# Performance work log

Hardware: AMD Instinct MI355X
Metric: run time of the kernel (lower is better)

## Reference

```python
import jax, jax.numpy as jnp
import numpy as np

N = 100000
E = 1600000
NFEAT = 128
NHID = 16
HEADS = 4
NCLASS = 40
NEG_SLOPE = 0.2
BN_EPS = 1e-5


def setup_inputs() -> dict:
    key = jax.random.key(0)
    ks = jax.random.split(key, 16)
    HC = NHID * HEADS  # 64
    x = jax.random.normal(ks[0], (N, NFEAT), dtype=jnp.float32)
    edge_index = jax.random.randint(ks[1], (2, E), 0, N, dtype=jnp.int64)
    def glorot(k, shape, fan_in):
        return jax.random.normal(k, shape, dtype=jnp.float32) * (1.0 / np.sqrt(fan_in))
    return {
        "x": x,
        "edge_index": edge_index,
        # layer 1: GATConv(NFEAT -> NHID, heads=HEADS, concat=True)
        "W1": glorot(ks[2], (NFEAT, HC), NFEAT),
        "att_src1": glorot(ks[3], (HEADS, NHID), NHID),
        "att_dst1": glorot(ks[4], (HEADS, NHID), NHID),
        "bias1": jnp.zeros((HC,), dtype=jnp.float32),
        # BatchNorm1d(HC), eval mode (running stats)
        "bn_gamma": jnp.ones((HC,), dtype=jnp.float32),
        "bn_beta": jnp.zeros((HC,), dtype=jnp.float32),
        "bn_mean": jax.random.normal(ks[5], (HC,), dtype=jnp.float32) * 0.1,
        "bn_var": jax.random.uniform(ks[6], (HC,), dtype=jnp.float32, minval=0.5, maxval=1.5),
        # layer 2: GATConv(HC -> NCLASS, heads=1, concat=False)
        "W2": glorot(ks[7], (HC, NCLASS), HC),
        "att_src2": glorot(ks[8], (1, NCLASS), NCLASS),
        "att_dst2": glorot(ks[9], (1, NCLASS), NCLASS),
        "bias2": jnp.zeros((NCLASS,), dtype=jnp.float32),
    }


def gat_conv(x, src, dst, W, att_src, att_dst, bias, concat):
    """PyG GATConv (eval; self-loops assumed already appended to src/dst)."""
    H, C = att_src.shape
    n = x.shape[0]
    h = (x @ W).reshape(n, H, C)                         # [N,H,C]
    a_s = (h * att_src[None]).sum(-1)                    # [N,H]
    a_d = (h * att_dst[None]).sum(-1)                    # [N,H]
    alpha = jax.nn.leaky_relu(a_s[src] + a_d[dst], NEG_SLOPE)  # [Et,H]
    # segment softmax over incoming edges of each destination node
    amax = jax.ops.segment_max(alpha, dst, num_segments=n)    # [N,H]
    ex = jnp.exp(alpha - amax[dst])
    denom = jax.ops.segment_sum(ex, dst, num_segments=n)
    coef = ex / denom[dst]                               # [Et,H]
    msg = h[src] * coef[:, :, None]                      # [Et,H,C]
    out = jax.ops.segment_sum(msg, dst, num_segments=n)  # [N,H,C]
    out = out.reshape(n, H * C) if concat else out.mean(axis=1)
    return out + bias


def reference(x, edge_index, W1, att_src1, att_dst1, bias1,
              bn_gamma, bn_beta, bn_mean, bn_var,
              W2, att_src2, att_dst2, bias2):
    n = x.shape[0]
    loops = jnp.arange(n, dtype=edge_index.dtype)
    src = jnp.concatenate([edge_index[0], loops])
    dst = jnp.concatenate([edge_index[1], loops])
    h = gat_conv(x, src, dst, W1, att_src1, att_dst1, bias1, concat=True)
    h = (h - bn_mean) * jax.lax.rsqrt(bn_var + BN_EPS) * bn_gamma + bn_beta
    h = jax.nn.relu(h)  # dropout is identity in eval
    out = gat_conv(h, src, dst, W2, att_src2, att_dst2, bias2, concat=False)
    return out
```

## Files before the change

kernel.cpp:

```cpp
#include <hip/hip_runtime.h>
#include <hip/hip_bf16.h>
#include <hip/hip_fp16.h>

#define NFEAT  128
#define HC     64
#define HEADS  4
#define NHID   16
#define NCLASS 40
#define NEG    0.2f
#define BN_EPS 1e-5f

#define BK_SH   9
#define CHUNK   8192
#define STAGE   12288

typedef _Float16 half8_t __attribute__((ext_vector_type(8)));
typedef _Float16 half4_t __attribute__((ext_vector_type(4)));
typedef float    f32x4_t __attribute__((ext_vector_type(4)));

__device__ __forceinline__ float leaky(float a) { return (a > 0.f) ? a : NEG * a; }

__global__ __launch_bounds__(256) void k_gemm1(
    const float* __restrict__ x, const float* __restrict__ W1,
    const float* __restrict__ att_s, const float* __restrict__ att_d,
    __half* __restrict__ h1, float* __restrict__ as1, float* __restrict__ ad1,
    int n)
{
    const int wave = threadIdx.x >> 6, lane = threadIdx.x & 63;
    const int quad = lane >> 4, l16 = lane & 15;

    half8_t bfrag[4][4];
    #pragma unroll
    for (int ks = 0; ks < 4; ++ks)
        #pragma unroll
        for (int ct = 0; ct < 4; ++ct)
            #pragma unroll
            for (int j = 0; j < 8; ++j)
                bfrag[ks][ct][j] =
                    (_Float16)W1[(ks * 32 + quad * 8 + j) * HC + ct * 16 + l16];

    float avs[4], avd[4];
    #pragma unroll
    for (int ct = 0; ct < 4; ++ct) {
        avs[ct] = att_s[ct * 16 + l16];
        avd[ct] = att_d[ct * 16 + l16];
    }

    const int nslab = (n + 15) >> 4;
    for (int slab = blockIdx.x * 4 + wave; slab < nslab; slab += gridDim.x * 4) {
        const int rowbase = slab * 16;
        const int arow = min(rowbase + l16, n - 1);
        const float* xp = x + (size_t)arow * NFEAT;

        f32x4_t acc[4] = {{0.f,0.f,0.f,0.f},{0.f,0.f,0.f,0.f},
                          {0.f,0.f,0.f,0.f},{0.f,0.f,0.f,0.f}};
        #pragma unroll
        for (int ks = 0; ks < 4; ++ks) {
            const float4 xa = *(const float4*)(xp + ks * 32 + quad * 8);
            const float4 xb = *(const float4*)(xp + ks * 32 + quad * 8 + 4);
            half8_t af;
            af[0] = (_Float16)xa.x; af[1] = (_Float16)xa.y;
            af[2] = (_Float16)xa.z; af[3] = (_Float16)xa.w;
            af[4] = (_Float16)xb.x; af[5] = (_Float16)xb.y;
            af[6] = (_Float16)xb.z; af[7] = (_Float16)xb.w;
            #pragma unroll
            for (int ct = 0; ct < 4; ++ct)
                acc[ct] = __builtin_amdgcn_mfma_f32_16x16x32_f16(
                    af, bfrag[ks][ct], acc[ct], 0, 0, 0);
        }

        #pragma unroll
        for (int reg = 0; reg < 4; ++reg) {
            const int row = rowbase + quad * 4 + reg;
            const bool valid = row < n;

            float4 ps, pd;
            ps.x = acc[0][reg] * avs[0]; pd.x = acc[0][reg] * avd[0];
            ps.y = acc[1][reg] * avs[1]; pd.y = acc[1][reg] * avd[1];
            ps.z = acc[2][reg] * avs[2]; pd.z = acc[2][reg] * avd[2];
            ps.w = acc[3][reg] * avs[3]; pd.w = acc[3][reg] * avd[3];
            #pragma unroll
            for (int off = 8; off >= 1; off >>= 1) {
                ps.x += __shfl_xor(ps.x, off, 64); pd.x += __shfl_xor(pd.x, off, 64);
                ps.y += __shfl_xor(ps.y, off, 64); pd.y += __shfl_xor(pd.y, off, 64);
                ps.z += __shfl_xor(ps.z, off, 64); pd.z += __shfl_xor(pd.z, off, 64);
                ps.w += __shfl_xor(ps.w, off, 64); pd.w += __shfl_xor(pd.w, off, 64);
            }
            if (valid) {
                #pragma unroll
                for (int ct = 0; ct < 4; ++ct)
                    h1[(size_t)row * HC + ct * 16 + l16] =
                        __float2half_rn(acc[ct][reg]);
                if (l16 == 0) {
                    *(float4*)(as1 + (size_t)row * HEADS) = ps;
                    *(float4*)(ad1 + (size_t)row * HEADS) = pd;
                }
            }
        }
    }
}

__global__ __launch_bounds__(512) void k_hist(
    const int* __restrict__ edst, int* __restrict__ hist, int E, int nbk)
{
    __shared__ int lh[256];
    const int w = blockIdx.x, t = threadIdx.x;
    for (int i = t; i < nbk; i += 512) lh[i] = 0;
    __syncthreads();
    const int lo = w * CHUNK, hi = min(E, lo + CHUNK);
    for (int e = lo + 4 * t; e < hi; e += 4 * 512) {
        const int4 d4 = *(const int4*)(edst + e);
        atomicAdd(&lh[d4.x >> BK_SH], 1);
        atomicAdd(&lh[d4.y >> BK_SH], 1);
        atomicAdd(&lh[d4.z >> BK_SH], 1);
        atomicAdd(&lh[d4.w >> BK_SH], 1);
    }
    __syncthreads();
    for (int i = t; i < nbk; i += 512) hist[(size_t)w * nbk + i] = lh[i];
}

__global__ __launch_bounds__(256) void k_colscan(
    int* __restrict__ hist, int* __restrict__ colsum, int nbk, int nw)
{
    __shared__ int wred[4];
    const int b = blockIdx.x, t = threadIdx.x;
    const int lane = t & 63, w = t >> 6;
    const int v = (t < nw) ? hist[(size_t)t * nbk + b] : 0;
    int sc = v;
    #pragma unroll
    for (int off = 1; off < 64; off <<= 1) {
        int u = __shfl_up(sc, off, 64);
        if (lane >= off) sc += u;
    }
    if (lane == 63) wred[w] = sc;
    __syncthreads();
    if (t == 0) { int a = 0; for (int i = 0; i < 4; ++i) { int xx = wred[i]; wred[i] = a; a += xx; } }
    __syncthreads();
    const int excl = sc - v + wred[w];
    if (t < nw) hist[(size_t)t * nbk + b] = excl;
    if (t == nw - 1) colsum[b] = excl + v;
}

__global__ __launch_bounds__(256) void k_bscan(
    const int* __restrict__ colsum, int* __restrict__ bstart, int nbk, int E)
{
    __shared__ int wred[4];
    const int t = threadIdx.x, lane = t & 63, w = t >> 6;
    const int v = (t < nbk) ? colsum[t] : 0;
    int sc = v;
    #pragma unroll
    for (int off = 1; off < 64; off <<= 1) {
        int u = __shfl_up(sc, off, 64);
        if (lane >= off) sc += u;
    }
    if (lane == 63) wred[w] = sc;
    __syncthreads();
    if (t == 0) { int a = 0; for (int i = 0; i < 4; ++i) { int xx = wred[i]; wred[i] = a; a += xx; } }
    __syncthreads();
    if (t < nbk) bstart[t] = sc - v + wred[w];
    if (t == 0) bstart[nbk] = E;
}

__global__ __launch_bounds__(512) void k_scatter(
    const int* __restrict__ esrc, const int* __restrict__ edst,
    const int* __restrict__ hist, const int* __restrict__ bstart,
    int2* __restrict__ pairs, int E, int nbk)
{
    __shared__ int cur[256];
    const int w = blockIdx.x, t = threadIdx.x;
    for (int i = t; i < nbk; i += 512)
        cur[i] = bstart[i] + hist[(size_t)w * nbk + i];
    __syncthreads();
    const int lo = w * CHUNK, hi = min(E, lo + CHUNK);
    for (int e = lo + 4 * t; e < hi; e += 4 * 512) {
        const int4 s4 = *(const int4*)(esrc + e);
        const int4 d4 = *(const int4*)(edst + e);
        int pos;
        pos = atomicAdd(&cur[d4.x >> BK_SH], 1); pairs[pos] = make_int2(s4.x, d4.x);
        pos = atomicAdd(&cur[d4.y >> BK_SH], 1); pairs[pos] = make_int2(s4.y, d4.y);
        pos = atomicAdd(&cur[d4.z >> BK_SH], 1); pairs[pos] = make_int2(s4.z, d4.z);
        pos = atomicAdd(&cur[d4.w >> BK_SH], 1); pairs[pos] = make_int2(s4.w, d4.w);
    }
}

__global__ __launch_bounds__(512) void k_build(
    const int2* __restrict__ pairs, const int* __restrict__ bstart,
    int* __restrict__ rowptr, int* __restrict__ csr, int n, int nbk)
{
    __shared__ int cnt[512];
    __shared__ int cur[512];
    __shared__ int stage[STAGE];
    __shared__ int wred[8];
    const int b = blockIdx.x, t = threadIdx.x;
    const int base = bstart[b], eend = bstart[b + 1], m = eend - base;
    const int n0 = b << BK_SH;
    const int nn = min(512, n - n0);

    cnt[t] = 0;
    __syncthreads();
    for (int e = base + t; e < eend; e += 512)
        atomicAdd(&cnt[pairs[e].y - n0], 1);
    __syncthreads();

    const int v = cnt[t];
    const int lane = t & 63, w = t >> 6;
    int sc = v;
    #pragma unroll
    for (int off = 1; off < 64; off <<= 1) {
        int u = __shfl_up(sc, off, 64);
        if (lane >= off) sc += u;
    }
    if (lane == 63) wred[w] = sc;
    __syncthreads();
    if (t == 0) { int a = 0; for (int i = 0; i < 8; ++i) { int xx = wred[i]; wred[i] = a; a += xx; } }
    __syncthreads();
    const int excl = sc - v + wred[w];
    cur[t] = excl;
    if (t < nn) rowptr[n0 + t] = base + excl + v;
    __syncthreads();

    for (int e = base + t; e < eend; e += 512) {
        const int2 p = pairs[e];
        const int loc = atomicAdd(&cur[p.y - n0], 1);
        if (loc < STAGE) stage[loc] = p.x;
        else             csr[base + loc] = p.x;
    }
    __syncthreads();
    const int lim = min(m, STAGE);
    for (int i = t; i < lim; i += 512) csr[base + i] = stage[i];
}

__global__ __launch_bounds__(256, 4) void k_agg1(
    const int* __restrict__ csr, const int* __restrict__ rowptr,
    const __half* __restrict__ h1, const float* __restrict__ as1,
    const float* __restrict__ ad1,
    const float* __restrict__ bias1, const float* __restrict__ gamma,
    const float* __restrict__ beta, const float* __restrict__ mean,
    const float* __restrict__ var,
    const float* __restrict__ W2, const float* __restrict__ ats2,
    const float* __restrict__ atd2,
    __half* __restrict__ g, float* __restrict__ as2o, float* __restrict__ ad2o,
    int n)
{
    __shared__ _Float16 sWh[NCLASS * HC];
    __shared__ float sh[16][68];
    __shared__ float sE[16][4][20];
    for (int i = threadIdx.x; i < NCLASS * HC; i += 256) sWh[i] = (_Float16)W2[i];
    __syncthreads();

    const int gi = threadIdx.x >> 4;
    const int q  = threadIdx.x & 15;
    const int myh = q >> 2;
    const unsigned nclamp = (unsigned)(n - 1);

    const float4 b1v = *(const float4*)(bias1 + 4 * q);
    const float4 gmv = *(const float4*)(gamma + 4 * q);
    const float4 vrv = *(const float4*)(var   + 4 * q);
    const float4 mnv = *(const float4*)(mean  + 4 * q);
    const float4 btv = *(const float4*)(beta  + 4 * q);
    float4 scv, shv;
    scv.x = gmv.x * rsqrtf(vrv.x + BN_EPS);
    scv.y = gmv.y * rsqrtf(vrv.y + BN_EPS);
    scv.z = gmv.z * rsqrtf(vrv.z + BN_EPS);
    scv.w = gmv.w * rsqrtf(vrv.w + BN_EPS);
    shv.x = btv.x - mnv.x * scv.x;
    shv.y = btv.y - mnv.y * scv.y;
    shv.z = btv.z - mnv.z * scv.z;
    shv.w = btv.w - mnv.w * scv.w;
    float4 at2 = {0.f, 0.f, 0.f, 0.f}, dt2 = {0.f, 0.f, 0.f, 0.f};
    if (q < 10) {
        at2 = *(const float4*)(ats2 + 4 * q);
        dt2 = *(const float4*)(atd2 + 4 * q);
    }

    for (int node0 = blockIdx.x * 16; node0 < n; node0 += gridDim.x * 16) {
        const int node = node0 + gi;
        if (node >= n) continue;

        const float4 adv = *(const float4*)(ad1 + node * HEADS);
        const float4 sv4 = *(const float4*)(as1 + node * HEADS);
        float4 eself;
        eself.x = __expf(leaky(sv4.x + adv.x));
        eself.y = __expf(leaky(sv4.y + adv.y));
        eself.z = __expf(leaky(sv4.z + adv.z));
        eself.w = __expf(leaky(sv4.w + adv.w));
        const float es = (myh == 0) ? eself.x : (myh == 1) ? eself.y
                       : (myh == 2) ? eself.z : eself.w;

        float4 acc;
        {
            const half4_t hv = *(const half4_t*)(h1 + (size_t)node * HC + 4 * q);
            acc.x = es * (float)hv[0]; acc.y = es * (float)hv[1];
            acc.z = es * (float)hv[2]; acc.w = es * (float)hv[3];
        }
        float4 dpart = {0.f, 0.f, 0.f, 0.f};

        const int start = (node == 0) ? 0 : rowptr[node - 1];
        const int end   = rowptr[node];

        for (int base = start; base < end; base += 16) {
            const int m = end - base;
            const int* cb = csr + base;

            const int myraw = cb[min(q, m - 1)];
            int idxs[16];
            #pragma unroll
            for (int e = 0; e < 16; ++e) idxs[e] = cb[e];

            half4_t wreg[16];
            #pragma unroll
            for (int e = 0; e < 16; ++e) {
                const unsigned off =
                    (min((unsigned)idxs[e], nclamp) << 7) + ((unsigned)q << 3);
                wreg[e] = *(const half4_t*)((const char*)h1 + off);
            }
            const float4 s4 =
                *(const float4*)(as1 + (size_t)min((unsigned)myraw, nclamp) * HEADS);
            __builtin_amdgcn_sched_barrier(0);

            const bool val = q < m;
            float4 ea;
            ea.x = val ? __expf(leaky(s4.x + adv.x)) : 0.f;
            ea.y = val ? __expf(leaky(s4.y + adv.y)) : 0.f;
            ea.z = val ? __expf(leaky(s4.z + adv.z)) : 0.f;
            ea.w = val ? __expf(leaky(s4.w + adv.w)) : 0.f;
            dpart.x += ea.x; dpart.y += ea.y;
            dpart.z += ea.z; dpart.w += ea.w;
            sE[gi][0][q] = ea.x;
            sE[gi][1][q] = ea.y;
            sE[gi][2][q] = ea.z;
            sE[gi][3][q] = ea.w;

            float eev[16];
            *(float4*)&eev[0]  = *(const float4*)&sE[gi][myh][0];
            *(float4*)&eev[4]  = *(const float4*)&sE[gi][myh][4];
            *(float4*)&eev[8]  = *(const float4*)&sE[gi][myh][8];
            *(float4*)&eev[12] = *(const float4*)&sE[gi][myh][12];

            #pragma unroll
            for (int e = 0; e < 16; ++e) {
                const float ee = eev[e];
                acc.x = fmaf((float)wreg[e][0], ee, acc.x);
                acc.y = fmaf((float)wreg[e][1], ee, acc.y);
                acc.z = fmaf((float)wreg[e][2], ee, acc.z);
                acc.w = fmaf((float)wreg[e][3], ee, acc.w);
            }
        }

        #pragma unroll
        for (int off = 8; off >= 1; off >>= 1) {
            dpart.x += __shfl_xor(dpart.x, off, 64);
            dpart.y += __shfl_xor(dpart.y, off, 64);
            dpart.z += __shfl_xor(dpart.z, off, 64);
            dpart.w += __shfl_xor(dpart.w, off, 64);
        }
        const float den = es + ((myh == 0) ? dpart.x : (myh == 1) ? dpart.y
                               : (myh == 2) ? dpart.z : dpart.w);
        const float rden = 1.f / den;

        float4 v;
        v.x = fmaxf(fmaf(acc.x * rden + b1v.x, scv.x, shv.x), 0.f);
        v.y = fmaxf(fmaf(acc.y * rden + b1v.y, scv.y, shv.y), 0.f);
        v.z = fmaxf(fmaf(acc.z * rden + b1v.z, scv.z, shv.z), 0.f);
        v.w = fmaxf(fmaf(acc.w * rden + b1v.w, scv.w, shv.w), 0.f);
        *(float4*)&sh[gi][4 * q] = v;

        float4 gacc = {0.f, 0.f, 0.f, 0.f};
        if (q < 10) {
            #pragma unroll 8
            for (int k = 0; k < HC; ++k) {
                const float hk = sh[gi][k];
                const half4_t wv = *(const half4_t*)&sWh[k * NCLASS + 4 * q];
                gacc.x = fmaf(hk, (float)wv[0], gacc.x);
                gacc.y = fmaf(hk, (float)wv[1], gacc.y);
                gacc.z = fmaf(hk, (float)wv[2], gacc.z);
                gacc.w = fmaf(hk, (float)wv[3], gacc.w);
            }
        }
        __half2 p0 = __float22half2_rn({gacc.x, gacc.y});
        __half2 p1 = __float22half2_rn({gacc.z, gacc.w});
        float2 packed; *(__half2*)&packed.x = p0; *(__half2*)&packed.y = p1;
        *(float2*)(g + (size_t)node * HC + 4 * q) = packed;

        float sv = gacc.x * at2.x + gacc.y * at2.y + gacc.z * at2.z + gacc.w * at2.w;
        float dv = gacc.x * dt2.x + gacc.y * dt2.y + gacc.z * dt2.z + gacc.w * dt2.w;
        #pragma unroll
        for (int off = 8; off >= 1; off >>= 1) {
            sv += __shfl_xor(sv, off, 64);
            dv += __shfl_xor(dv, off, 64);
        }
        if (q == 0) { as2o[node] = sv; ad2o[node] = dv; }
    }
}

__global__ __launch_bounds__(256, 4) void k_agg2(
    const int* __restrict__ csr, const int* __restrict__ rowptr,
    const __half* __restrict__ g, const float* __restrict__ as2,
    const float* __restrict__ ad2, const float* __restrict__ bias2,
    float* __restrict__ out, int n)
{
    __shared__ float sE[16][20];
    const int gi = threadIdx.x >> 4;
    const int q  = threadIdx.x & 15;
    const unsigned nclamp = (unsigned)(n - 1);

    float4 b2v = {0.f, 0.f, 0.f, 0.f};
    if (q < 10) b2v = *(const float4*)(bias2 + 4 * q);

    for (int node0 = blockIdx.x * 16; node0 < n; node0 += gridDim.x * 16) {
        const int node = node0 + gi;
        if (node >= n) continue;

        const float ad2d = ad2[node];
        const float eself = __expf(leaky(as2[node] + ad2d));

        float4 acc;
        {
            const half4_t hv = *(const half4_t*)(g + (size_t)node * HC + 4 * q);
            acc.x = eself * (float)hv[0]; acc.y = eself * (float)hv[1];
            acc.z = eself * (float)hv[2]; acc.w = eself * (float)hv[3];
        }
        float dpart = 0.f;

        const int start = (node == 0) ? 0 : rowptr[node - 1];
        const int end   = rowptr[node];

        for (int base = start; base < end; base += 16) {
            const int m = end - base;
            const int* cb = csr + base;

            const int myraw = cb[min(q, m - 1)];
            int idxs[16];
            #pragma unroll
            for (int e = 0; e < 16; ++e) idxs[e] = cb[e];

            half4_t wreg[16];
            #pragma unroll
            for (int e = 0; e < 16; ++e) {
                const unsigned off =
                    (min((unsigned)idxs[e], nclamp) << 7) + ((unsigned)q << 3);
                wreg[e] = *(const half4_t*)((const char*)g + off);
            }
            const float sca = as2[min((unsigned)myraw, nclamp)];
            __builtin_amdgcn_sched_barrier(0);

            const float ea = (q < m) ? __expf(leaky(sca + ad2d)) : 0.f;
            dpart += ea;
            sE[gi][q] = ea;

            float eev[16];
            *(float4*)&eev[0]  = *(const float4*)&sE[gi][0];
            *(float4*)&eev[4]  = *(const float4*)&sE[gi][4];
            *(float4*)&eev[8]  = *(const float4*)&sE[gi][8];
            *(float4*)&eev[12] = *(const float4*)&sE[gi][12];

            #pragma unroll
            for (int e = 0; e < 16; ++e) {
                const float ee = eev[e];
                acc.x = fmaf((float)wreg[e][0], ee, acc.x);
                acc.y = fmaf((float)wreg[e][1], ee, acc.y);
                acc.z = fmaf((float)wreg[e][2], ee, acc.z);
                acc.w = fmaf((float)wreg[e][3], ee, acc.w);
            }
        }

        #pragma unroll
        for (int off = 8; off >= 1; off >>= 1)
            dpart += __shfl_xor(dpart, off, 64);
        const float rden = 1.f / (dpart + eself);

        if (q < 10) {
            float4 r;
            r.x = acc.x * rden + b2v.x;
            r.y = acc.y * rden + b2v.y;
            r.z = acc.z * rden + b2v.z;
            r.w = acc.w * rden + b2v.w;
            *(float4*)(out + (size_t)node * NCLASS + 4 * q) = r;
        }
    }
}

extern "C" void kernel_launch(void* const* d_in, const int* in_sizes, int n_in,
                              void* d_out, int out_size, void* d_ws, size_t ws_size,
                              hipStream_t stream)
{
    const float* x    = (const float*)d_in[0];
    const int*   ei   = (const int*)  d_in[1];
    const float* W1   = (const float*)d_in[2];
    const float* as1w = (const float*)d_in[3];
    const float* ad1w = (const float*)d_in[4];
    const float* b1   = (const float*)d_in[5];
    const float* gm   = (const float*)d_in[6];
    const float* bt   = (const float*)d_in[7];
    const float* mn   = (const float*)d_in[8];
    const float* vr   = (const float*)d_in[9];
    const float* W2   = (const float*)d_in[10];
    const float* as2w = (const float*)d_in[11];
    const float* ad2w = (const float*)d_in[12];
    const float* b2   = (const float*)d_in[13];

    const int n = in_sizes[0] / NFEAT;
    const int E = in_sizes[1] / 2;
    const int* esrc = ei;
    const int* edst = ei + E;

    const int nbk = (n + 511) >> BK_SH;
    const int nw  = (E + CHUNK - 1) / CHUNK;

    float*  ws   = (float*)d_ws;
    __half* h1   = (__half*)ws;
    float*  a_s1 = ws   + (size_t)n * 32;
    float*  a_d1 = a_s1 + (size_t)n * 4;
    __half* gbuf = (__half*)(a_d1 + (size_t)n * 4);
    float*  a_s2 = a_d1 + (size_t)n * 4 + (size_t)n * 32;
    float*  a_d2 = a_s2 + n;
    int2*   pairs  = (int2*)(a_d2 + n);
    int*    csr    = (int*)(pairs + E);
    int*    rowptr = csr + E;
    int*    hist   = rowptr + n;
    int*    colsum = hist + (size_t)nw * nbk;
    int*    bstart = colsum + nbk;
    float*  outv = (float*)d_out;

    const int nblk = 2048;

    k_hist   <<<nw, 512, 0, stream>>>(edst, hist, E, nbk);
    k_colscan<<<nbk, 256, 0, stream>>>(hist, colsum, nbk, nw);
    k_bscan  <<<1, 256, 0, stream>>>(colsum, bstart, nbk, E);
    k_scatter<<<nw, 512, 0, stream>>>(esrc, edst, hist, bstart, pairs, E, nbk);
    k_build  <<<nbk, 512, 0, stream>>>(pairs, bstart, rowptr, csr, n, nbk);
    k_gemm1  <<<512, 256, 0, stream>>>(x, W1, as1w, ad1w, h1, a_s1, a_d1, n);
    k_agg1   <<<nblk, 256, 0, stream>>>(csr, rowptr, h1, a_s1, a_d1,
                                        b1, gm, bt, mn, vr,
                                        W2, as2w, ad2w, gbuf, a_s2, a_d2, n);
    k_agg2   <<<nblk, 256, 0, stream>>>(csr, rowptr, gbuf, a_s2, a_d2,
                                        b2, outv, n);
}
```

Before: 265.6 us.

## Bucket nodes by degree class and process aggregation in degree-sorted order

Classifies each node by incoming-edge count into four classes of 16-edge steps, builds a permutation that groups nodes of the same class, and has both aggregation kernels walk nodes through that permutation. The aim is less intra-wavefront imbalance, since the 16-node groups in a block would then have similar loop trip counts. It adds two small kernels, an extra indirection per node, and loses the sequential locality of node-indexed loads and stores.

```diff
diff --git a/kernel.cpp b/kernel.cpp
--- a/kernel.cpp
+++ b/kernel.cpp
@@ -142,10 +142,12 @@
 }
 
 __global__ __launch_bounds__(256) void k_bscan(
-    const int* __restrict__ colsum, int* __restrict__ bstart, int nbk, int E)
+    const int* __restrict__ colsum, int* __restrict__ bstart,
+    int* __restrict__ clsbuf, int nbk, int E)
 {
     __shared__ int wred[4];
     const int t = threadIdx.x, lane = t & 63, w = t >> 6;
+    if (t < 8) clsbuf[t] = 0;
     const int v = (t < nbk) ? colsum[t] : 0;
     int sc = v;
     #pragma unroll
@@ -185,18 +187,21 @@
 
 __global__ __launch_bounds__(512) void k_build(
     const int2* __restrict__ pairs, const int* __restrict__ bstart,
-    int* __restrict__ rowptr, int* __restrict__ csr, int n, int nbk)
+    int* __restrict__ rowptr, int* __restrict__ csr, int* __restrict__ clsbuf,
+    int n, int nbk)
 {
     __shared__ int cnt[512];
     __shared__ int cur[512];
     __shared__ int stage[STAGE];
     __shared__ int wred[8];
+    __shared__ int lcls[4];
     const int b = blockIdx.x, t = threadIdx.x;
     const int base = bstart[b], eend = bstart[b + 1], m = eend - base;
     const int n0 = b << BK_SH;
     const int nn = min(512, n - n0);
 
     cnt[t] = 0;
+    if (t < 4) lcls[t] = 0;
     __syncthreads();
     for (int e = base + t; e < eend; e += 512)
         atomicAdd(&cnt[pairs[e].y - n0], 1);
@@ -216,8 +221,12 @@
     __syncthreads();
     const int excl = sc - v + wred[w];
     cur[t] = excl;
-    if (t < nn) rowptr[n0 + t] = base + excl + v;
-    __syncthreads();
+    if (t < nn) {
+        rowptr[n0 + t] = base + excl + v;
+        atomicAdd(&lcls[min(3, (v + 15) >> 4)], 1);
+    }
+    __syncthreads();
+    if (t < 4) atomicAdd(&clsbuf[t], lcls[t]);
 
     for (int e = base + t; e < eend; e += 512) {
         const int2 p = pairs[e];
@@ -230,7 +239,44 @@
     for (int i = t; i < lim; i += 512) csr[base + i] = stage[i];
 }
 
+__global__ void k_clsinit(int* __restrict__ clsbuf)
+{
+    if (threadIdx.x == 0) {
+        int a = 0;
+        for (int i = 0; i < 4; ++i) { const int c = clsbuf[i]; clsbuf[4 + i] = a; a += c; }
+    }
+}
+
+__global__ __launch_bounds__(256) void k_perms(
+    const int* __restrict__ rowptr, int* __restrict__ clsbuf,
+    int* __restrict__ perm, int n)
+{
+    __shared__ int lcnt[4], lbase[4], lcur[4];
+    const int t = threadIdx.x;
+    const int node = blockIdx.x * 256 + t;
+    if (t < 4) lcnt[t] = 0;
+    __syncthreads();
+    int cls = 0;
+    if (node < n) {
+        const int start = (node == 0) ? 0 : rowptr[node - 1];
+        const int deg = rowptr[node] - start;
+        cls = min(3, (deg + 15) >> 4);
+        atomicAdd(&lcnt[cls], 1);
+    }
+    __syncthreads();
+    if (t < 4) {
+        lbase[t] = atomicAdd(&clsbuf[4 + t], lcnt[t]);
+        lcur[t] = 0;
+    }
+    __syncthreads();
+    if (node < n) {
+        const int r = atomicAdd(&lcur[cls], 1);
+        perm[lbase[cls] + r] = node;
+    }
+}
+
 __global__ __launch_bounds__(256, 4) void k_agg1(
+    const int* __restrict__ perm,
     const int* __restrict__ csr, const int* __restrict__ rowptr,
     const __half* __restrict__ h1, const float* __restrict__ as1,
     const float* __restrict__ ad1,
@@ -274,8 +320,9 @@
     }
 
     for (int node0 = blockIdx.x * 16; node0 < n; node0 += gridDim.x * 16) {
-        const int node = node0 + gi;
-        if (node >= n) continue;
+        const int pos = node0 + gi;
+        if (pos >= n) continue;
+        const int node = perm[pos];
 
         const float4 adv = *(const float4*)(ad1 + node * HEADS);
         const float4 sv4 = *(const float4*)(as1 + node * HEADS);
@@ -394,6 +441,7 @@
 }
 
 __global__ __launch_bounds__(256, 4) void k_agg2(
+    const int* __restrict__ perm,
     const int* __restrict__ csr, const int* __restrict__ rowptr,
     const __half* __restrict__ g, const float* __restrict__ as2,
     const float* __restrict__ ad2, const float* __restrict__ bias2,
@@ -408,8 +456,9 @@
     if (q < 10) b2v = *(const float4*)(bias2 + 4 * q);
 
     for (int node0 = blockIdx.x * 16; node0 < n; node0 += gridDim.x * 16) {
-        const int node = node0 + gi;
-        if (node >= n) continue;
+        const int pos = node0 + gi;
+        if (pos >= n) continue;
+        const int node = perm[pos];
 
         const float ad2d = ad2[node];
         const float eself = __expf(leaky(as2[node] + ad2d));
@@ -520,19 +569,24 @@
     int*    hist   = rowptr + n;
     int*    colsum = hist + (size_t)nw * nbk;
     int*    bstart = colsum + nbk;
+    int*    clsbuf = bstart + nbk + 1;
+    int*    perm   = clsbuf + 8;
     float*  outv = (float*)d_out;
 
     const int nblk = 2048;
+    const int npb  = (n + 255) / 256;
 
     k_hist   <<<nw, 512, 0, stream>>>(edst, hist, E, nbk);
     k_colscan<<<nbk, 256, 0, stream>>>(hist, colsum, nbk, nw);
-    k_bscan  <<<1, 256, 0, stream>>>(colsum, bstart, nbk, E);
+    k_bscan  <<<1, 256, 0, stream>>>(colsum, bstart, clsbuf, nbk, E);
     k_scatter<<<nw, 512, 0, stream>>>(esrc, edst, hist, bstart, pairs, E, nbk);
-    k_build  <<<nbk, 512, 0, stream>>>(pairs, bstart, rowptr, csr, n, nbk);
+    k_build  <<<nbk, 512, 0, stream>>>(pairs, bstart, rowptr, csr, clsbuf, n, nbk);
+    k_clsinit<<<1, 64, 0, stream>>>(clsbuf);
+    k_perms  <<<npb, 256, 0, stream>>>(rowptr, clsbuf, perm, n);
     k_gemm1  <<<512, 256, 0, stream>>>(x, W1, as1w, ad1w, h1, a_s1, a_d1, n);
-    k_agg1   <<<nblk, 256, 0, stream>>>(csr, rowptr, h1, a_s1, a_d1,
+    k_agg1   <<<nblk, 256, 0, stream>>>(perm, csr, rowptr, h1, a_s1, a_d1,
                                         b1, gm, bt, mn, vr,
                                         W2, as2w, ad2w, gbuf, a_s2, a_d2, n);
-    k_agg2   <<<nblk, 256, 0, stream>>>(csr, rowptr, gbuf, a_s2, a_d2,
+    k_agg2   <<<nblk, 256, 0, stream>>>(perm, csr, rowptr, gbuf, a_s2, a_d2,
                                         b2, outv, n);
 }
```

Result: no change. 269.4 us (+1.4%).
